# Optimization experiments

Measured on AMD Instinct MI355X. Metric: run time of the kernel, lower is better.

The kernel has to match this reference:

```python
import jax, jax.numpy as jnp
import numpy as np

DIM, QK, GS, DEPTH, VOCAB, ROT = 16, 128, 256, 8, 1024, 32
EPS = 1e-5


def scale_norm(x, g):
    # ScaleNorm: x / max(||x|| * dim^-0.5, eps) * g
    norm = jnp.linalg.norm(x, axis=-1, keepdims=True) * (DIM ** -0.5)
    return x / jnp.clip(norm, EPS) * g


def rotate_half(x):
    # interleaved pairs: (x0,x1,x2,x3,...) -> (-x1,x0,-x3,x2,...)
    xr = x.reshape(x.shape[:-1] + (-1, 2))
    a, b = xr[..., 0], xr[..., 1]
    return jnp.stack((-b, a), axis=-1).reshape(x.shape)


def apply_rotary(x, cos, sin):
    # rotary applied to first ROT dims only
    xr, xp = x[..., :ROT], x[..., ROT:]
    return jnp.concatenate([xr * cos + rotate_half(xr) * sin, xp], axis=-1)


def flash_layer(x, p, cos, sin, keymask, n):
    b = x.shape[0]
    normed = scale_norm(x, p['norm_g'])
    # shift_tokens: first half of channels shifted forward by one position
    xs, xp = jnp.split(normed, 2, axis=-1)
    xs = jnp.pad(xs, ((0, 0), (1, 0), (0, 0)))[:, :-1]
    normed = jnp.concatenate([xs, xp], axis=-1)
    hid = jax.nn.silu(normed @ p['Wh'] + p['bh'])  # [b,n,64]
    v, gate = jnp.split(hid, 2, axis=-1)           # each [b,n,32]
    qk = jax.nn.silu(normed @ p['Wqk'] + p['bqk'])  # [b,n,128]
    offs = qk[..., None, :] * p['gamma'] + p['beta']  # [b,n,4,128]
    quad_q, lin_q, quad_k, lin_k = [apply_rotary(offs[..., i, :], cos, sin) for i in range(4)]
    pad = (-n) % GS
    grp = lambda t: jnp.pad(t, ((0, 0), (0, pad), (0, 0))).reshape(b, -1, GS, t.shape[-1])
    quad_q, quad_k, lin_q, lin_k, vg = map(grp, (quad_q, quad_k, lin_q, lin_k, v))
    # quadratic (local, within-group) attention with ReLU^2
    sim = jnp.einsum('bgid,bgjd->bgij', quad_q, quad_k) / GS
    attn = jnp.square(jax.nn.relu(sim)) * keymask  # mask out padded keys
    quad_out = jnp.einsum('bgij,bgjd->bgid', attn, vg)
    # linear (global, across-group) attention, reduced over groups
    lin_kv = jnp.einsum('bgnd,bgne->bde', lin_k, vg) / n
    lin_out = jnp.einsum('bgnd,bde->bgne', lin_q, lin_kv)
    out = (quad_out + lin_out).reshape(b, -1, v.shape[-1])[:, :n]
    out = gate * out
    return out @ p['Wo'] + p['bo'] + x


def forward(kmer_data, token_emb, pos_scale, norm_g, Wh, bh, Wqk, bqk, gamma, beta, Wo, bo, final_g, Wl, bl, W1, b1, W2, b2):
    b, n = kmer_data.shape
    x = token_emb[kmer_data]  # [b,n,16]
    t = jnp.arange(n, dtype=jnp.float32)
    # ScaledSinuEmbedding
    inv = 1.0 / (10000.0 ** (jnp.arange(0, DIM, 2, dtype=jnp.float32) / DIM))
    sinu = t[:, None] * inv[None, :]
    pos = jnp.concatenate([jnp.sin(sinu), jnp.cos(sinu)], axis=-1) * pos_scale
    x = x + pos
    # rotary tables (dim 32, interleaved repeat)
    rinv = 1.0 / (10000.0 ** (jnp.arange(0, ROT, 2, dtype=jnp.float32) / ROT))
    rf = jnp.repeat(t[:, None] * rinv[None, :], 2, axis=-1)  # [n,32]
    cos, sin = jnp.cos(rf), jnp.sin(rf)
    # key mask for padded positions (996 -> 1024)
    pad = (-n) % GS
    keymask = jnp.pad(jnp.ones((n,), jnp.float32), (0, pad)).reshape(1, -1, 1, GS)
    for i in range(DEPTH):
        p = dict(norm_g=norm_g[i], Wh=Wh[i], bh=bh[i], Wqk=Wqk[i], bqk=bqk[i],
                 gamma=gamma[i], beta=beta[i], Wo=Wo[i], bo=bo[i])
        x = flash_layer(x, p, cos, sin, keymask, n)
    logits = scale_norm(x, final_g) @ Wl + bl  # [b,n,1024]
    h = jnp.max(logits, axis=-1)               # AdaptiveMaxPool1d(1) + Flatten -> [b,n]
    h = jax.nn.relu(h @ W1 + b1)
    return h @ W2 + b2                          # [b,1]


def setup_inputs() -> dict:
    key = jax.random.key(0)
    ks = jax.random.split(key, 12)
    r = lambda k, shape, s: jax.random.normal(k, shape, jnp.float32) * s
    return {
        'kmer_data': jax.random.randint(ks[0], (128, 996), 0, VOCAB),
        'token_emb': r(ks[1], (VOCAB, DIM), 1.0),
        'pos_scale': jnp.float32(1.0),
        'norm_g': jnp.ones((DEPTH,), jnp.float32),
        'Wh': r(ks[2], (DEPTH, DIM, 64), 0.1),
        'bh': jnp.zeros((DEPTH, 64), jnp.float32),
        'Wqk': r(ks[3], (DEPTH, DIM, QK), 0.1),
        'bqk': jnp.zeros((DEPTH, QK), jnp.float32),
        'gamma': 1.0 + r(ks[4], (DEPTH, 4, QK), 0.02),
        'beta': r(ks[5], (DEPTH, 4, QK), 0.02),
        'Wo': r(ks[6], (DEPTH, 32, DIM), 0.1),
        'bo': jnp.zeros((DEPTH, DIM), jnp.float32),
        'final_g': jnp.float32(1.0),
        'Wl': r(ks[7], (DIM, VOCAB), 0.1),
        'bl': jnp.zeros((VOCAB,), jnp.float32),
        'W1': r(ks[8], (996, 32), 0.05),
        'b1': jnp.zeros((32,), jnp.float32),
        'W2': r(ks[9], (32, 1), 0.1),
        'b2': jnp.zeros((1,), jnp.float32),
    }


def reference(kmer_data, token_emb, pos_scale, norm_g, Wh, bh, Wqk, bqk, gamma, beta, Wo, bo, final_g, Wl, bl, W1, b1, W2, b2):
    return forward(kmer_data, token_emb, pos_scale, norm_g, Wh, bh, Wqk, bqk,
                   gamma, beta, Wo, bo, final_g, Wl, bl, W1, b1, W2, b2)
```

## Files before the change

kernel.cpp:

```cpp
#include <hip/hip_runtime.h>

typedef short s16x8 __attribute__((ext_vector_type(8)));
typedef float f32x4 __attribute__((ext_vector_type(4)));

#define NB    128
#define NTOK  996
#define NPAD  1024
#define NGRP  4
#define GSZ   256
#define NLAY  8

__device__ __forceinline__ float bf2f(unsigned short u){
    unsigned int v = ((unsigned int)u) << 16;
    return __uint_as_float(v);
}
__device__ __forceinline__ unsigned short f2bf(float f){
    unsigned int x = __float_as_uint(f);
    unsigned int r = (x + 0x7fffu + ((x >> 16) & 1u)) >> 16;
    return (unsigned short)r;
}
__device__ __forceinline__ unsigned int packbf(float a, float b){
    return (unsigned int)f2bf(a) | ((unsigned int)f2bf(b) << 16);
}
__device__ __forceinline__ float silu(float v){
    return v / (1.0f + __expf(-v));
}

__device__ __forceinline__ s16x8 derive_core(const unsigned short* __restrict__ qrow, int d0,
        float4 g0, float4 g1, float4 b0, float4 b1,
        const float* __restrict__ rp, bool rot){
    uint4 u = *(const uint4*)(qrow + d0);
    float y0 = bf2f((unsigned short)(u.x & 0xffffu))*g0.x + b0.x;
    float y1 = bf2f((unsigned short)(u.x >> 16))    *g0.y + b0.y;
    float y2 = bf2f((unsigned short)(u.y & 0xffffu))*g0.z + b0.z;
    float y3 = bf2f((unsigned short)(u.y >> 16))    *g0.w + b0.w;
    float y4 = bf2f((unsigned short)(u.z & 0xffffu))*g1.x + b1.x;
    float y5 = bf2f((unsigned short)(u.z >> 16))    *g1.y + b1.y;
    float y6 = bf2f((unsigned short)(u.w & 0xffffu))*g1.z + b1.z;
    float y7 = bf2f((unsigned short)(u.w >> 16))    *g1.w + b1.w;
    if (rot){
        float4 c4 = *(const float4*)(rp);
        float4 s4 = *(const float4*)(rp + 16);
        float a;
        a = y0; y0 = a*c4.x - y1*s4.x; y1 = y1*c4.x + a*s4.x;
        a = y2; y2 = a*c4.y - y3*s4.y; y3 = y3*c4.y + a*s4.y;
        a = y4; y4 = a*c4.z - y5*s4.z; y5 = y5*c4.z + a*s4.z;
        a = y6; y6 = a*c4.w - y7*s4.w; y7 = y7*c4.w + a*s4.w;
    }
    union { unsigned int uu[4]; s16x8 s; } r;
    r.uu[0] = packbf(y0, y1);
    r.uu[1] = packbf(y2, y3);
    r.uu[2] = packbf(y4, y5);
    r.uu[3] = packbf(y6, y7);
    return r.s;
}

__global__ void k_rope(float* __restrict__ rope){
    int t = blockIdx.x * 256 + threadIdx.x;
    if (t >= NPAD) return;
    float tf = (float)t;
    #pragma unroll
    for (int i = 0; i < 16; i++){
        float inv = expf(((float)(2*i) / 32.0f) * -9.210340371976184f);
        float ang = tf * inv;
        rope[t*32 + i]      = cosf(ang);
        rope[t*32 + 16 + i] = sinf(ang);
    }
}

__global__ __launch_bounds__(256) void k_embed(const int* __restrict__ kmer,
                                               const float* __restrict__ emb,
                                               const float* __restrict__ ps,
                                               float* __restrict__ x){
    int gid = blockIdx.x * 256 + threadIdx.x;
    if (gid >= NB * NTOK) return;
    int b = gid / NTOK;
    int tt = gid - b * NTOK;
    int idx = kmer[gid];
    const float* er = emb + (size_t)idx * 16;
    float pscale = ps[0];
    float tf = (float)tt;
    float* xr = x + (size_t)gid * 16;
    #pragma unroll
    for (int i = 0; i < 8; i++){
        float inv = expf(((float)(2*i) / 16.0f) * -9.210340371976184f);
        float ang = tf * inv;
        xr[i]     = er[i]     + sinf(ang) * pscale;
        xr[8 + i] = er[8 + i] + cosf(ang) * pscale;
    }
}

__global__ __launch_bounds__(256, 2) void k_pre(const float* __restrict__ x,
                                             const float* __restrict__ Wh, const float* __restrict__ bh,
                                             const float* __restrict__ Wqk, const float* __restrict__ bqk,
                                             const float* __restrict__ norm_g,
                                             const float* __restrict__ gamma, const float* __restrict__ beta,
                                             const float* __restrict__ rope, int layer,
                                             unsigned short* __restrict__ qk,
                                             unsigned short* __restrict__ vT,
                                             unsigned short* __restrict__ gateb,
                                             float* __restrict__ linkvp){
    __shared__ __align__(16) unsigned short WcT[192 * 40];
    __shared__ __align__(16) unsigned short As[256 * 40];
    __shared__ unsigned int nrm[256][4];
    __shared__ __align__(16) unsigned short LkT[128 * 72];
    __shared__ __align__(16) unsigned short Vt[32 * 72];
    int tid = threadIdx.x;
    int qt = blockIdx.x & 3, b = blockIdx.x >> 2;
    const float* Whl = Wh  + (size_t)layer * 1024;
    const float* Wql = Wqk + (size_t)layer * 2048;
    const float* gLin = gamma + (size_t)layer * 512 + 384;
    const float* bLin = beta  + (size_t)layer * 512 + 384;
    for (int i = tid; i < 1024; i += 256){ int d = i >> 6, c = i & 63;  WcT[c*40 + d] = f2bf(Whl[i]); }
    for (int i = tid; i < 2048; i += 256){ int d = i >> 7, c = i & 127; WcT[(64 + c)*40 + d] = f2bf(Wql[i]); }
    if (tid < 192){
        int i = tid;
        float bv = (i < 64) ? bh[layer*64 + i] : bqk[layer*128 + (i - 64)];
        WcT[i*40 + 16] = f2bf(bv);
        WcT[i*40 + 17] = 0;
        unsigned int* zz = (unsigned int*)(WcT + i*40 + 18);
        #pragma unroll
        for (int k = 0; k < 7; k++) zz[k] = 0u;
    }
    int tt = qt*256 + tid;
    int tsafe = tt < NTOK ? tt : (NTOK - 1);
    float g = norm_g[layer];
    unsigned int* dd = (unsigned int*)(As + tid * 40);
    {
        const float4* xr4 = (const float4*)(x + ((size_t)b*NTOK + tsafe) * 16);
        float cur[16];
        float s2 = 0.f;
        #pragma unroll
        for (int c = 0; c < 4; c++){
            float4 v4 = xr4[c];
            cur[4*c] = v4.x; cur[4*c+1] = v4.y; cur[4*c+2] = v4.z; cur[4*c+3] = v4.w;
        }
        #pragma unroll
        for (int d = 0; d < 16; d++) s2 += cur[d]*cur[d];
        float sc = g / fmaxf(sqrtf(s2) * 0.25f, 1e-5f);
        #pragma unroll
        for (int i = 0; i < 4; i++) nrm[tid][i] = packbf(cur[2*i]*sc, cur[2*i+1]*sc);
        #pragma unroll
        for (int i = 0; i < 4; i++) dd[4 + i] = packbf(cur[8 + 2*i]*sc, cur[9 + 2*i]*sc);
        dd[8] = 0x00003f80u;
        #pragma unroll
        for (int i = 9; i < 16; i++) dd[i] = 0u;
    }
    __syncthreads();
    if (tt == 0){
        #pragma unroll
        for (int i = 0; i < 4; i++) dd[i] = 0u;
    } else if (tid > 0){
        #pragma unroll
        for (int i = 0; i < 4; i++) dd[i] = nrm[tid - 1][i];
    } else {
        const float4* xp4 = (const float4*)(x + ((size_t)b*NTOK + tt - 1) * 16);
        float prv[16]; float p2 = 0.f;
        #pragma unroll
        for (int c = 0; c < 4; c++){
            float4 v4 = xp4[c];
            prv[4*c] = v4.x; prv[4*c+1] = v4.y; prv[4*c+2] = v4.z; prv[4*c+3] = v4.w;
        }
        #pragma unroll
        for (int d = 0; d < 16; d++) p2 += prv[d]*prv[d];
        float sp = g / fmaxf(sqrtf(p2) * 0.25f, 1e-5f);
        #pragma unroll
        for (int i = 0; i < 4; i++) dd[i] = packbf(prv[2*i]*sp, prv[2*i+1]*sp);
    }
    __syncthreads();
    int w = tid >> 6, lane = tid & 63, m16 = lane & 15, quad = lane >> 4;
    s16x8 wf[12];
    #pragma unroll
    for (int mi = 0; mi < 12; mi++)
        wf[mi] = *(const s16x8*)(WcT + (mi*16 + m16)*40 + quad*8);
    f32x4 zacc = {0.f,0.f,0.f,0.f};
    f32x4 lacc[2][2] = {{{0,0,0,0},{0,0,0,0}},{{0,0,0,0},{0,0,0,0}}};
    #pragma unroll
    for (int nt = 0; nt < 4; nt++){
        int tloc = w*64 + nt*16 + m16;
        int ttk = qt*256 + tloc;
        bool tv = ttk < NTOK;
        int c = w*16 + m16;
        s16x8 bf = *(const s16x8*)(As + tloc*40 + quad*8);
        size_t rowq = ((size_t)b*NPAD + ttk);
        #pragma unroll
        for (int mi = 0; mi < 12; mi++){
            f32x4 r = __builtin_amdgcn_mfma_f32_16x16x32_bf16(wf[mi], bf, zacc, 0, 0, 0);
            float sv[4];
            #pragma unroll
            for (int reg = 0; reg < 4; reg++) sv[reg] = silu(r[reg]);
            int wc0 = mi*16 + quad*4;
            if (mi < 2){
                #pragma unroll
                for (int reg = 0; reg < 4; reg++){
                    unsigned short pv = tv ? f2bf(sv[reg]) : (unsigned short)0;
                    vT[((size_t)b*32 + wc0 + reg)*NPAD + ttk] = pv;
                    Vt[(wc0 + reg)*72 + c] = pv;
                }
            } else if (mi < 4){
                *(uint2*)(gateb + rowq*32 + (wc0 - 32)) = make_uint2(packbf(sv[0],sv[1]), packbf(sv[2],sv[3]));
            } else {
                int qd = wc0 - 64;
                *(uint2*)(qk + rowq*128 + qd) = make_uint2(packbf(sv[0],sv[1]), packbf(sv[2],sv[3]));
                float y0 = sv[0]*gLin[qd]   + bLin[qd];
                float y1 = sv[1]*gLin[qd+1] + bLin[qd+1];
                float y2 = sv[2]*gLin[qd+2] + bLin[qd+2];
                float y3 = sv[3]*gLin[qd+3] + bLin[qd+3];
                if (qd < 32){
                    const float* rp = rope + ttk*32 + (qd >> 1);
                    float c0 = rp[0], s0 = rp[16], c1 = rp[1], s1 = rp[17];
                    float a;
                    a = y0; y0 = a*c0 - y1*s0; y1 = y1*c0 + a*s0;
                    a = y2; y2 = a*c1 - y3*s1; y3 = y3*c1 + a*s1;
                }
                LkT[(qd+0)*72 + c] = f2bf(y0);
                LkT[(qd+1)*72 + c] = f2bf(y1);
                LkT[(qd+2)*72 + c] = f2bf(y2);
                LkT[(qd+3)*72 + c] = f2bf(y3);
            }
        }
        __syncthreads();
        #pragma unroll
        for (int ks2 = 0; ks2 < 2; ks2++){
            s16x8 a0 = *(const s16x8*)(LkT + ((2*w  )*16 + m16)*72 + ks2*32 + quad*8);
            s16x8 a1 = *(const s16x8*)(LkT + ((2*w+1)*16 + m16)*72 + ks2*32 + quad*8);
            s16x8 b0 = *(const s16x8*)(Vt + (m16)*72 + ks2*32 + quad*8);
            s16x8 b1 = *(const s16x8*)(Vt + (16 + m16)*72 + ks2*32 + quad*8);
            lacc[0][0] = __builtin_amdgcn_mfma_f32_16x16x32_bf16(a0, b0, lacc[0][0], 0,0,0);
            lacc[0][1] = __builtin_amdgcn_mfma_f32_16x16x32_bf16(a0, b1, lacc[0][1], 0,0,0);
            lacc[1][0] = __builtin_amdgcn_mfma_f32_16x16x32_bf16(a1, b0, lacc[1][0], 0,0,0);
            lacc[1][1] = __builtin_amdgcn_mfma_f32_16x16x32_bf16(a1, b1, lacc[1][1], 0,0,0);
        }
        __syncthreads();
    }
    const float invn = 1.0f / 996.0f;
    #pragma unroll
    for (int i = 0; i < 2; i++){
        #pragma unroll
        for (int j = 0; j < 2; j++){
            int e = j*16 + m16;
            #pragma unroll
            for (int reg = 0; reg < 4; reg++){
                int d = (2*w + i)*16 + quad*4 + reg;
                linkvp[(((size_t)qt*NB + b)*32 + e)*128 + d] = lacc[i][j][reg] * invn;
            }
        }
    }
}

#define KD_BYTES (64*136*2)
#define PW_BYTES (8*16*72*2)
__global__ __launch_bounds__(512, 2) void k_quad(const unsigned short* __restrict__ qk,
                                              const unsigned short* __restrict__ vT,
                                              const unsigned short* __restrict__ gateb,
                                              const float* __restrict__ linkvp,
                                              const float* __restrict__ rope,
                                              const float* __restrict__ gamma, const float* __restrict__ beta,
                                              int layer,
                                              const float* __restrict__ Wo, const float* __restrict__ bo,
                                              float* __restrict__ x){
    __shared__ __align__(16) unsigned char smem[KD_BYTES + PW_BYTES];
    __shared__ __align__(16) unsigned short LkBs[32 * 136];
    __shared__ float sWo[512];
    __shared__ float sbo[16];
    unsigned short* Kd = (unsigned short*)smem;
    unsigned short* Pw = (unsigned short*)(smem + KD_BYTES);
    int tid = threadIdx.x;
    int blk = blockIdx.x;
    int g = blk & 3, b = blk >> 2;
    int tg0 = g * GSZ;
    const float* gamL = gamma + (size_t)layer * 512;
    const float* betL = beta  + (size_t)layer * 512;
    sWo[tid] = Wo[layer*512 + tid];
    if (tid < 16) sbo[tid] = bo[layer*16 + tid];

    int w = tid >> 6, lane = tid & 63, m16 = lane & 15, quad = lane >> 4;

    int tqA = tg0 + w*32 + m16;
    int tqB = tqA + 16;
    const unsigned short* qrowA = qk + ((size_t)b*NPAD + tqA)*128;
    const unsigned short* qrowB = qk + ((size_t)b*NPAD + tqB)*128;
    const float* rpA = rope + tqA*32 + quad*4;
    const float* rpB = rope + tqB*32 + quad*4;
    s16x8 qf[2][4];
    #pragma unroll
    for (int ks = 0; ks < 4; ks++){
        int d0 = ks*32 + quad*8;
        float4 g0 = *(const float4*)(gamL + d0), g1 = *(const float4*)(gamL + d0 + 4);
        float4 b0 = *(const float4*)(betL + d0), b1 = *(const float4*)(betL + d0 + 4);
        bool rot = (ks == 0) && (quad < 4);
        qf[0][ks] = derive_core(qrowA, d0, g0,g1,b0,b1, rpA, rot);
        qf[1][ks] = derive_core(qrowB, d0, g0,g1,b0,b1, rpB, rot);
    }

    const float* gK = gamL + 256;
    const float* bK = betL + 256;
    f32x4 oacc[2][2] = {{{0,0,0,0},{0,0,0,0}},{{0,0,0,0},{0,0,0,0}}};
    unsigned short* myP = Pw + w*16*72;

    for (int ch = 0; ch < 4; ch++){
        __syncthreads();
        {
            int r = tid >> 3, seg = (tid & 7) * 16;
            int tk = tg0 + ch*64 + r;
            const unsigned short* krow = qk + ((size_t)b*NPAD + tk)*128 + seg;
            unsigned int* dst = (unsigned int*)(Kd + r*136 + seg);
            #pragma unroll
            for (int h = 0; h < 2; h++){
                uint4 u = ((const uint4*)krow)[h];
                unsigned int uu[4] = {u.x, u.y, u.z, u.w};
                float y[8];
                #pragma unroll
                for (int k = 0; k < 4; k++){
                    int d = h*8 + 2*k;
                    y[2*k]   = bf2f((unsigned short)(uu[k] & 0xffffu)) * gK[seg + d]     + bK[seg + d];
                    y[2*k+1] = bf2f((unsigned short)(uu[k] >> 16))     * gK[seg + d + 1] + bK[seg + d + 1];
                }
                if (seg < 32){
                    const float* rp = rope + tk*32 + (seg >> 1) + h*4;
                    #pragma unroll
                    for (int p = 0; p < 4; p++){
                        float c = rp[p], s = rp[16 + p];
                        float a = y[2*p], d = y[2*p+1];
                        y[2*p]   = a*c - d*s;
                        y[2*p+1] = d*c + a*s;
                    }
                }
                #pragma unroll
                for (int k = 0; k < 4; k++) dst[h*4 + k] = packbf(y[2*k], y[2*k+1]);
            }
        }
        __syncthreads();
        #pragma unroll
        for (int i = 0; i < 2; i++){
            #pragma unroll
            for (int np = 0; np < 2; np++){
                f32x4 s0 = {0,0,0,0}, s1 = {0,0,0,0};
                #pragma unroll
                for (int ks = 0; ks < 4; ks++){
                    s16x8 kf0 = *(const s16x8*)(Kd + ((np*2  )*16 + m16)*136 + ks*32 + quad*8);
                    s16x8 kf1 = *(const s16x8*)(Kd + ((np*2+1)*16 + m16)*136 + ks*32 + quad*8);
                    s0 = __builtin_amdgcn_mfma_f32_16x16x32_bf16(qf[i][ks], kf0, s0, 0,0,0);
                    s1 = __builtin_amdgcn_mfma_f32_16x16x32_bf16(qf[i][ks], kf1, s1, 0,0,0);
                }
                #pragma unroll
                for (int j = 0; j < 2; j++){
                    int kl = (np*2 + j)*16 + m16;
                    bool kv = (tg0 + ch*64 + kl) < NTOK;
                    #pragma unroll
                    for (int reg = 0; reg < 4; reg++){
                        float a = fmaxf(j ? s1[reg] : s0[reg], 0.0f);
                        a = a * a;
                        myP[(quad*4 + reg)*72 + kl] = kv ? f2bf(a) : (unsigned short)0;
                    }
                }
            }
            #pragma unroll
            for (int ks = 0; ks < 2; ks++){
                s16x8 pa = *(const s16x8*)(myP + m16*72 + ks*32 + quad*8);
                s16x8 vf0 = *(const s16x8*)(vT + ((size_t)b*32 + m16)*NPAD + tg0 + ch*64 + ks*32 + quad*8);
                s16x8 vf1 = *(const s16x8*)(vT + ((size_t)b*32 + 16 + m16)*NPAD + tg0 + ch*64 + ks*32 + quad*8);
                oacc[i][0] = __builtin_amdgcn_mfma_f32_16x16x32_bf16(pa, vf0, oacc[i][0], 0,0,0);
                oacc[i][1] = __builtin_amdgcn_mfma_f32_16x16x32_bf16(pa, vf1, oacc[i][1], 0,0,0);
            }
        }
    }
    const float qsc = 1.0f / 65536.0f;
    #pragma unroll
    for (int i = 0; i < 2; i++)
        #pragma unroll
        for (int j = 0; j < 2; j++)
            oacc[i][j] = oacc[i][j] * qsc;
    {
        int e = tid >> 4, dbase = (tid & 15) * 8;
        float s[8];
        #pragma unroll
        for (int k = 0; k < 8; k++) s[k] = 0.f;
        #pragma unroll
        for (int part = 0; part < 4; part++){
            const float* src = linkvp + (((size_t)part*NB + b)*32 + e)*128 + dbase;
            float4 u0 = *(const float4*)src;
            float4 u1 = *(const float4*)(src + 4);
            s[0]+=u0.x; s[1]+=u0.y; s[2]+=u0.z; s[3]+=u0.w;
            s[4]+=u1.x; s[5]+=u1.y; s[6]+=u1.z; s[7]+=u1.w;
        }
        unsigned int* dst = (unsigned int*)(LkBs + e*136 + dbase);
        #pragma unroll
        for (int k = 0; k < 4; k++) dst[k] = packbf(s[2*k], s[2*k+1]);
    }
    __syncthreads();
    {
        const float* gamQ = gamL + 128;
        const float* betQ = betL + 128;
        #pragma unroll
        for (int ks = 0; ks < 4; ks++){
            int d0 = ks*32 + quad*8;
            float4 g0 = *(const float4*)(gamQ + d0), g1 = *(const float4*)(gamQ + d0 + 4);
            float4 b0 = *(const float4*)(betQ + d0), b1 = *(const float4*)(betQ + d0 + 4);
            bool rot = (ks == 0) && (quad < 4);
            s16x8 lf0 = derive_core(qrowA, d0, g0,g1,b0,b1, rpA, rot);
            s16x8 lf1 = derive_core(qrowB, d0, g0,g1,b0,b1, rpB, rot);
            #pragma unroll
            for (int j = 0; j < 2; j++){
                s16x8 lb = *(const s16x8*)(LkBs + (j*16 + m16)*136 + ks*32 + quad*8);
                oacc[0][j] = __builtin_amdgcn_mfma_f32_16x16x32_bf16(lf0, lb, oacc[0][j], 0,0,0);
                oacc[1][j] = __builtin_amdgcn_mfma_f32_16x16x32_bf16(lf1, lb, oacc[1][j], 0,0,0);
            }
        }
    }
    float* Obw = (float*)smem + w*1056;
    #pragma unroll
    for (int i = 0; i < 2; i++)
        #pragma unroll
        for (int j = 0; j < 2; j++)
            #pragma unroll
            for (int reg = 0; reg < 4; reg++)
                Obw[(i*16 + quad*4 + reg)*33 + j*16 + m16] = oacc[i][j][reg];
    {
        int r = lane >> 1, dp = (lane & 1) * 8;
        int p = tg0 + w*32 + r;
        if (p < NTOK){
            const unsigned short* gr = gateb + ((size_t)b*NPAD + p)*32;
            float* xr = x + ((size_t)b * NTOK + p)*16 + dp;
            float4 x0 = *(const float4*)xr;
            float4 x1 = *(const float4*)(xr + 4);
            float a[8] = { sbo[dp]+x0.x, sbo[dp+1]+x0.y, sbo[dp+2]+x0.z, sbo[dp+3]+x0.w,
                           sbo[dp+4]+x1.x, sbo[dp+5]+x1.y, sbo[dp+6]+x1.z, sbo[dp+7]+x1.w };
            #pragma unroll
            for (int eh = 0; eh < 4; eh++){
                uint4 gu = *(const uint4*)(gr + eh*8);
                unsigned int gg[4] = {gu.x, gu.y, gu.z, gu.w};
                #pragma unroll
                for (int k = 0; k < 4; k++){
                    float gv0 = bf2f((unsigned short)(gg[k] & 0xffffu));
                    float gv1 = bf2f((unsigned short)(gg[k] >> 16));
                    int e = eh*8 + 2*k;
                    float ov0 = Obw[r*33 + e] * gv0;
                    float ov1 = Obw[r*33 + e + 1] * gv1;
                    const float* wr0 = &sWo[e*16 + dp];
                    const float* wr1 = &sWo[(e+1)*16 + dp];
                    #pragma unroll
                    for (int kk = 0; kk < 8; kk++) a[kk] += ov0 * wr0[kk] + ov1 * wr1[kk];
                }
            }
            *(float4*)xr = make_float4(a[0],a[1],a[2],a[3]);
            *(float4*)(xr+4) = make_float4(a[4],a[5],a[6],a[7]);
        }
    }
}

__global__ __launch_bounds__(256) void k_head(const float* __restrict__ x,
                                              const float* __restrict__ Wl, const float* __restrict__ bl,
                                              const float* __restrict__ fg, float* __restrict__ h){
    __shared__ __align__(16) unsigned short WlT[512 * 40];
    __shared__ __align__(16) unsigned short As[64 * 40];
    int tid = threadIdx.x;
    int gid0 = blockIdx.x * 64;
    if (tid < 64){
        int t = gid0 + tid;
        const float4* xr4 = (const float4*)(x + (size_t)t * 16);
        float cur[16]; float s2 = 0.f;
        #pragma unroll
        for (int c = 0; c < 4; c++){
            float4 v4 = xr4[c];
            cur[4*c] = v4.x; cur[4*c+1] = v4.y; cur[4*c+2] = v4.z; cur[4*c+3] = v4.w;
        }
        #pragma unroll
        for (int d = 0; d < 16; d++) s2 += cur[d]*cur[d];
        float sc = fg[0] / fmaxf(sqrtf(s2) * 0.25f, 1e-5f);
        unsigned int* dd = (unsigned int*)(As + tid * 40);
        #pragma unroll
        for (int i = 0; i < 8; i++) dd[i] = packbf(cur[2*i]*sc, cur[2*i+1]*sc);
        dd[8] = 0x00003f80u;
        #pragma unroll
        for (int i = 9; i < 16; i++) dd[i] = 0u;
    }
    int w = tid >> 6, lane = tid & 63, m16 = lane & 15, quad = lane >> 4;
    float vm0 = -3e38f, vm1 = -3e38f, vm2 = -3e38f, vm3 = -3e38f;
    for (int half = 0; half < 2; half++){
        __syncthreads();
        for (int i = tid; i < 8192; i += 256){
            int d = i >> 9, c = i & 511;
            WlT[c*40 + d] = f2bf(Wl[(size_t)d*1024 + half*512 + c]);
        }
        for (int i = tid; i < 512; i += 256){
            WlT[i*40 + 16] = f2bf(bl[half*512 + i]);
            WlT[i*40 + 17] = 0;
            unsigned int* zz = (unsigned int*)(WlT + i*40 + 18);
            #pragma unroll
            for (int k = 0; k < 7; k++) zz[k] = 0u;
        }
        __syncthreads();
        s16x8 af = *(const s16x8*)(As + (w*16 + m16)*40 + quad*8);
        f32x4 zacc = {0,0,0,0};
        for (int nt = 0; nt < 32; nt++){
            s16x8 bf = *(const s16x8*)(WlT + (nt*16 + m16)*40 + quad*8);
            f32x4 r = __builtin_amdgcn_mfma_f32_16x16x32_bf16(af, bf, zacc, 0,0,0);
            vm0 = fmaxf(vm0, r[0]);
            vm1 = fmaxf(vm1, r[1]);
            vm2 = fmaxf(vm2, r[2]);
            vm3 = fmaxf(vm3, r[3]);
        }
    }
    #pragma unroll
    for (int off = 1; off < 16; off <<= 1){
        vm0 = fmaxf(vm0, __shfl_xor(vm0, off, 64));
        vm1 = fmaxf(vm1, __shfl_xor(vm1, off, 64));
        vm2 = fmaxf(vm2, __shfl_xor(vm2, off, 64));
        vm3 = fmaxf(vm3, __shfl_xor(vm3, off, 64));
    }
    if (m16 == 0){
        int t0 = gid0 + w*16 + quad*4;
        h[t0 + 0] = vm0;
        h[t0 + 1] = vm1;
        h[t0 + 2] = vm2;
        h[t0 + 3] = vm3;
    }
}

__global__ __launch_bounds__(256) void k_final(const float* __restrict__ h,
                                               const float* __restrict__ W1, const float* __restrict__ b1,
                                               const float* __restrict__ W2, const float* __restrict__ b2,
                                               float* __restrict__ out){
    int b = blockIdx.x;
    int tid = threadIdx.x;
    int j = tid & 31, part = tid >> 5;
    float acc = 0.f;
    for (int i = part; i < NTOK; i += 8)
        acc += h[(size_t)b*NTOK + i] * W1[(size_t)i*32 + j];
    __shared__ float red[8][33];
    red[part][j] = acc;
    __syncthreads();
    if (tid < 32){
        float s = b1[tid];
        #pragma unroll
        for (int p = 0; p < 8; p++) s += red[p][tid];
        s = fmaxf(s, 0.f);
        red[0][tid] = s * W2[tid];
    }
    __syncthreads();
    if (tid == 0){
        float s = b2[0];
        #pragma unroll
        for (int jj = 0; jj < 32; jj++) s += red[0][jj];
        out[b] = s;
    }
}

extern "C" void kernel_launch(void* const* d_in, const int* in_sizes, int n_in,
                              void* d_out, int out_size, void* d_ws, size_t ws_size,
                              hipStream_t stream){
    const int*   kmer  = (const int*)d_in[0];
    const float* emb   = (const float*)d_in[1];
    const float* ps    = (const float*)d_in[2];
    const float* ng    = (const float*)d_in[3];
    const float* Wh    = (const float*)d_in[4];
    const float* bh    = (const float*)d_in[5];
    const float* Wqk   = (const float*)d_in[6];
    const float* bqk   = (const float*)d_in[7];
    const float* gamma = (const float*)d_in[8];
    const float* beta  = (const float*)d_in[9];
    const float* Wo    = (const float*)d_in[10];
    const float* bo    = (const float*)d_in[11];
    const float* fg    = (const float*)d_in[12];
    const float* Wl    = (const float*)d_in[13];
    const float* bl    = (const float*)d_in[14];
    const float* W1    = (const float*)d_in[15];
    const float* b1    = (const float*)d_in[16];
    const float* W2    = (const float*)d_in[17];
    const float* b2    = (const float*)d_in[18];
    float* out = (float*)d_out;

    char* wsp = (char*)d_ws;
    float* x = (float*)wsp;                     wsp += (size_t)NB*NTOK*16*4;
    unsigned short* qk = (unsigned short*)wsp;  wsp += (size_t)NB*NPAD*128*2;
    unsigned short* vT = (unsigned short*)wsp;  wsp += (size_t)NB*32*NPAD*2;
    unsigned short* gateb = (unsigned short*)wsp; wsp += (size_t)NB*NPAD*32*2;
    float* linkvp = (float*)wsp;                wsp += (size_t)4*NB*32*128*4;
    float* rope = (float*)wsp;                  wsp += (size_t)NPAD*32*4;
    float* h = (float*)wsp;                     wsp += (size_t)NB*NTOK*4;

    k_rope<<<4, 256, 0, stream>>>(rope);
    k_embed<<<(NB*NTOK + 255)/256, 256, 0, stream>>>(kmer, emb, ps, x);
    for (int layer = 0; layer < NLAY; layer++){
        k_pre<<<NB*4, 256, 0, stream>>>(x, Wh, bh, Wqk, bqk, ng, gamma, beta, rope, layer, qk, vT, gateb, linkvp);
        k_quad<<<NB*NGRP, 512, 0, stream>>>(qk, vT, gateb, linkvp, rope, gamma, beta, layer, Wo, bo, x);
    }
    k_head<<<NB*NTOK/64, 256, 0, stream>>>(x, Wl, bl, fg, h);
    k_final<<<NB, 256, 0, stream>>>(h, W1, b1, W2, b2, out);
}
```

Before: 811.9 us.

## Double-buffer LkT/Vt in k_pre, prefetch V fragments, widen k_head tiles

```diff
diff --git a/kernel.cpp b/kernel.cpp
--- a/kernel.cpp
+++ b/kernel.cpp
@@ -101,10 +101,9 @@
                                              unsigned short* __restrict__ gateb,
                                              float* __restrict__ linkvp){
     __shared__ __align__(16) unsigned short WcT[192 * 40];
-    __shared__ __align__(16) unsigned short As[256 * 40];
     __shared__ unsigned int nrm[256][4];
-    __shared__ __align__(16) unsigned short LkT[128 * 72];
-    __shared__ __align__(16) unsigned short Vt[32 * 72];
+    __shared__ __align__(16) unsigned char arena[2 * 23040];
+    unsigned short* As = (unsigned short*)arena;
     int tid = threadIdx.x;
     int qt = blockIdx.x & 3, b = blockIdx.x >> 2;
     const float* Whl = Wh  + (size_t)layer * 1024;
@@ -173,19 +172,25 @@
     #pragma unroll
     for (int mi = 0; mi < 12; mi++)
         wf[mi] = *(const s16x8*)(WcT + (mi*16 + m16)*40 + quad*8);
+    s16x8 bfr[4];
+    #pragma unroll
+    for (int nt = 0; nt < 4; nt++)
+        bfr[nt] = *(const s16x8*)(As + ((w*64 + nt*16 + m16))*40 + quad*8);
+    __syncthreads();
     f32x4 zacc = {0.f,0.f,0.f,0.f};
     f32x4 lacc[2][2] = {{{0,0,0,0},{0,0,0,0}},{{0,0,0,0},{0,0,0,0}}};
     #pragma unroll
     for (int nt = 0; nt < 4; nt++){
+        unsigned short* LkT = (unsigned short*)(arena + (nt & 1) * 23040);
+        unsigned short* Vt  = (unsigned short*)(arena + (nt & 1) * 23040 + 18432);
         int tloc = w*64 + nt*16 + m16;
         int ttk = qt*256 + tloc;
         bool tv = ttk < NTOK;
         int c = w*16 + m16;
-        s16x8 bf = *(const s16x8*)(As + tloc*40 + quad*8);
         size_t rowq = ((size_t)b*NPAD + ttk);
         #pragma unroll
         for (int mi = 0; mi < 12; mi++){
-            f32x4 r = __builtin_amdgcn_mfma_f32_16x16x32_bf16(wf[mi], bf, zacc, 0, 0, 0);
+            f32x4 r = __builtin_amdgcn_mfma_f32_16x16x32_bf16(wf[mi], bfr[nt], zacc, 0, 0, 0);
             float sv[4];
             #pragma unroll
             for (int reg = 0; reg < 4; reg++) sv[reg] = silu(r[reg]);
@@ -231,7 +236,6 @@
             lacc[1][0] = __builtin_amdgcn_mfma_f32_16x16x32_bf16(a1, b0, lacc[1][0], 0,0,0);
             lacc[1][1] = __builtin_amdgcn_mfma_f32_16x16x32_bf16(a1, b1, lacc[1][1], 0,0,0);
         }
-        __syncthreads();
     }
     const float invn = 1.0f / 996.0f;
     #pragma unroll
@@ -300,6 +304,12 @@
 
     for (int ch = 0; ch < 4; ch++){
         __syncthreads();
+        s16x8 vf[2][2];
+        #pragma unroll
+        for (int ks = 0; ks < 2; ks++)
+            #pragma unroll
+            for (int j = 0; j < 2; j++)
+                vf[ks][j] = *(const s16x8*)(vT + ((size_t)b*32 + j*16 + m16)*NPAD + tg0 + ch*64 + ks*32 + quad*8);
         {
             int r = tid >> 3, seg = (tid & 7) * 16;
             int tk = tg0 + ch*64 + r;
@@ -358,10 +368,8 @@
             #pragma unroll
             for (int ks = 0; ks < 2; ks++){
                 s16x8 pa = *(const s16x8*)(myP + m16*72 + ks*32 + quad*8);
-                s16x8 vf0 = *(const s16x8*)(vT + ((size_t)b*32 + m16)*NPAD + tg0 + ch*64 + ks*32 + quad*8);
-                s16x8 vf1 = *(const s16x8*)(vT + ((size_t)b*32 + 16 + m16)*NPAD + tg0 + ch*64 + ks*32 + quad*8);
-                oacc[i][0] = __builtin_amdgcn_mfma_f32_16x16x32_bf16(pa, vf0, oacc[i][0], 0,0,0);
-                oacc[i][1] = __builtin_amdgcn_mfma_f32_16x16x32_bf16(pa, vf1, oacc[i][1], 0,0,0);
+                oacc[i][0] = __builtin_amdgcn_mfma_f32_16x16x32_bf16(pa, vf[ks][0], oacc[i][0], 0,0,0);
+                oacc[i][1] = __builtin_amdgcn_mfma_f32_16x16x32_bf16(pa, vf[ks][1], oacc[i][1], 0,0,0);
             }
         }
     }
@@ -453,10 +461,10 @@
                                               const float* __restrict__ Wl, const float* __restrict__ bl,
                                               const float* __restrict__ fg, float* __restrict__ h){
     __shared__ __align__(16) unsigned short WlT[512 * 40];
-    __shared__ __align__(16) unsigned short As[64 * 40];
+    __shared__ __align__(16) unsigned short As[256 * 40];
     int tid = threadIdx.x;
-    int gid0 = blockIdx.x * 64;
-    if (tid < 64){
+    int gid0 = blockIdx.x * 256;
+    {
         int t = gid0 + tid;
         const float4* xr4 = (const float4*)(x + (size_t)t * 16);
         float cur[16]; float s2 = 0.f;
@@ -476,7 +484,9 @@
         for (int i = 9; i < 16; i++) dd[i] = 0u;
     }
     int w = tid >> 6, lane = tid & 63, m16 = lane & 15, quad = lane >> 4;
-    float vm0 = -3e38f, vm1 = -3e38f, vm2 = -3e38f, vm3 = -3e38f;
+    f32x4 vm[4];
+    #pragma unroll
+    for (int i = 0; i < 4; i++) vm[i] = (f32x4){-3e38f,-3e38f,-3e38f,-3e38f};
     for (int half = 0; half < 2; half++){
         __syncthreads();
         for (int i = tid; i < 8192; i += 256){
@@ -491,30 +501,39 @@
             for (int k = 0; k < 7; k++) zz[k] = 0u;
         }
         __syncthreads();
-        s16x8 af = *(const s16x8*)(As + (w*16 + m16)*40 + quad*8);
+        s16x8 af[4];
+        #pragma unroll
+        for (int i = 0; i < 4; i++)
+            af[i] = *(const s16x8*)(As + (w*64 + i*16 + m16)*40 + quad*8);
         f32x4 zacc = {0,0,0,0};
         for (int nt = 0; nt < 32; nt++){
             s16x8 bf = *(const s16x8*)(WlT + (nt*16 + m16)*40 + quad*8);
-            f32x4 r = __builtin_amdgcn_mfma_f32_16x16x32_bf16(af, bf, zacc, 0,0,0);
-            vm0 = fmaxf(vm0, r[0]);
-            vm1 = fmaxf(vm1, r[1]);
-            vm2 = fmaxf(vm2, r[2]);
-            vm3 = fmaxf(vm3, r[3]);
-        }
-    }
-    #pragma unroll
-    for (int off = 1; off < 16; off <<= 1){
-        vm0 = fmaxf(vm0, __shfl_xor(vm0, off, 64));
-        vm1 = fmaxf(vm1, __shfl_xor(vm1, off, 64));
-        vm2 = fmaxf(vm2, __shfl_xor(vm2, off, 64));
-        vm3 = fmaxf(vm3, __shfl_xor(vm3, off, 64));
+            #pragma unroll
+            for (int i = 0; i < 4; i++){
+                f32x4 r = __builtin_amdgcn_mfma_f32_16x16x32_bf16(af[i], bf, zacc, 0,0,0);
+                #pragma unroll
+                for (int reg = 0; reg < 4; reg++)
+                    vm[i][reg] = fmaxf(vm[i][reg], r[reg]);
+            }
+        }
+    }
+    #pragma unroll
+    for (int i = 0; i < 4; i++){
+        #pragma unroll
+        for (int off = 1; off < 16; off <<= 1){
+            #pragma unroll
+            for (int reg = 0; reg < 4; reg++)
+                vm[i][reg] = fmaxf(vm[i][reg], __shfl_xor(vm[i][reg], off, 64));
+        }
     }
     if (m16 == 0){
-        int t0 = gid0 + w*16 + quad*4;
-        h[t0 + 0] = vm0;
-        h[t0 + 1] = vm1;
-        h[t0 + 2] = vm2;
-        h[t0 + 3] = vm3;
+        #pragma unroll
+        for (int i = 0; i < 4; i++){
+            int t0 = gid0 + w*64 + i*16 + quad*4;
+            #pragma unroll
+            for (int reg = 0; reg < 4; reg++)
+                h[t0 + reg] = vm[i][reg];
+        }
     }
 }
 
@@ -586,6 +605,6 @@
         k_pre<<<NB*4, 256, 0, stream>>>(x, Wh, bh, Wqk, bqk, ng, gamma, beta, rope, layer, qk, vT, gateb, linkvp);
         k_quad<<<NB*NGRP, 512, 0, stream>>>(qk, vT, gateb, linkvp, rope, gamma, beta, layer, Wo, bo, x);
     }
-    k_head<<<NB*NTOK/64, 256, 0, stream>>>(x, Wl, bl, fg, h);
+    k_head<<<NB*NTOK/256, 256, 0, stream>>>(x, Wl, bl, fg, h);
     k_final<<<NB, 256, 0, stream>>>(h, W1, b1, W2, b2, out);
 }
```

Measured after the change: 826.0 us. No clear change (+1.7%).
